# Optimization experiments

Measured on AMD Instinct MI355X. Metric: run time of the kernel, lower is better.

## Reference

```python
import jax, jax.numpy as jnp
import numpy as np

POPULATION = 1000000.0  # __init__ arg of MarkovChainRNN_Model
B, T, F = 16384, 2048, 2  # batch, timesteps, (beta, gamma) per step


def setup_inputs() -> dict:
    key = jax.random.key(0)
    k1, k2 = jax.random.split(key)
    # per-step (beta, gamma) rates in [0, 1)
    inputs = jax.random.uniform(k1, (B, T, F), dtype=jnp.float32)
    # initial [S, I, R] state; scaled so S+I+R is O(population)
    initial_state = jax.random.uniform(k2, (B, 3), dtype=jnp.float32) * POPULATION
    return {"inputs": inputs, "initial_state": initial_state}


def reference(inputs, initial_state):
    # SIR cell update, one step per day:
    #   new_inf = beta * S * I / N ; new_rec = gamma * I
    #   S' = S - new_inf ; I' = I + new_inf - new_rec ; R' = R + new_rec
    # Keras RNN(cell, return_state=True) -> (last_output, last_state);
    # for an SIR cell output == state, so both returns are the final state.
    def step(state, u):
        beta, gamma = u[:, 0], u[:, 1]            # [B], [B]
        S, I, R = state[:, 0], state[:, 1], state[:, 2]
        new_inf = beta * S * I / POPULATION
        new_rec = gamma * I
        new_state = jnp.stack([S - new_inf,
                               I + new_inf - new_rec,
                               R + new_rec], axis=-1)  # [B, 3]
        return new_state, None

    xs = jnp.transpose(inputs, (1, 0, 2))  # time-major [T, B, F]
    final_state, _ = jax.lax.scan(step, initial_state, xs)
    return (final_state, final_state)
```

## Files before the change

### kernel.cpp

```cpp
#include <hip/hip_runtime.h>
#include <stdint.h>
#include <stddef.h>


#define T_STEPS 2048
#define C_STEPS 64
#define NCHUNK  (T_STEPS / C_STEPS)
#define BPB     64
#define PAIRS   (C_STEPS / 2)
#define INSTR_PER_CHUNK 32

#define INV_POP 1e-6f

__device__ __forceinline__ void stage_chunk(const float* __restrict__ in,
                                            float4* lds, int b0, int c, int lane)
{
    const int hi = lane >> 5;
    const int q  = lane & 31;
#pragma unroll
    for (int j = 0; j < INSTR_PER_CHUNK; ++j) {
        const int bi = 2 * j + hi;
        const int p  = q ^ (bi & 15);
        const float* g = in
            + (size_t)(b0 + bi) * (T_STEPS * 2)
            + (size_t)c * (C_STEPS * 2)
            + (size_t)(p * 4);
        float4* l = lds + j * 64;
        __builtin_amdgcn_global_load_lds(
            (__attribute__((address_space(1))) void*)g,
            (__attribute__((address_space(3))) void*)l,
            16, 0, 0);
    }
}

__device__ __forceinline__ void compute_chunk(const float4* lds, int tid,
                                              float& S, float& I, float& R)
{
    const int swz = tid & 15;
    const float4* row = lds + tid * PAIRS;
#pragma unroll
    for (int p = 0; p < PAIRS; ++p) {
        const float4 v = row[p ^ swz];

        float ni = S * I * (v.x * INV_POP);
        float nr = v.y * I;
        S = S - ni;
        I = I + ni - nr;
        R = R + nr;

        ni = S * I * (v.z * INV_POP);
        nr = v.w * I;
        S = S - ni;
        I = I + ni - nr;
        R = R + nr;
    }
}

__global__ __launch_bounds__(64)
void sir_scan_kernel(const float* __restrict__ in, const float* __restrict__ init,
                     float* __restrict__ out, int half)
{
    __shared__ float4 bufA[BPB * PAIRS];
    __shared__ float4 bufB[BPB * PAIRS];

    const int tid = threadIdx.x;
    const int b0  = blockIdx.x * BPB;
    const int gb  = b0 + tid;

    float S = init[gb * 3 + 0];
    float I = init[gb * 3 + 1];
    float R = init[gb * 3 + 2];

    stage_chunk(in, bufA, b0, 0, tid);

#pragma unroll 1
    for (int c = 0; c < NCHUNK; c += 2) {
        asm volatile("s_waitcnt vmcnt(0)" ::: "memory");
        if (c + 1 < NCHUNK) stage_chunk(in, bufB, b0, c + 1, tid);
        compute_chunk(bufA, tid, S, I, R);

        asm volatile("s_waitcnt vmcnt(0)" ::: "memory");
        if (c + 2 < NCHUNK) stage_chunk(in, bufA, b0, c + 2, tid);
        compute_chunk(bufB, tid, S, I, R);
    }

    out[gb * 3 + 0] = S;
    out[gb * 3 + 1] = I;
    out[gb * 3 + 2] = R;
    out[half + gb * 3 + 0] = S;
    out[half + gb * 3 + 1] = I;
    out[half + gb * 3 + 2] = R;
}

extern "C" void kernel_launch(void* const* d_in, const int* in_sizes, int n_in,
                              void* d_out, int out_size, void* d_ws, size_t ws_size,
                              hipStream_t stream) {
    (void)in_sizes; (void)n_in; (void)d_ws; (void)ws_size;
    const float* in   = (const float*)d_in[0];
    const float* init = (const float*)d_in[1];
    float* out        = (float*)d_out;
    const int half = out_size / 2;

    dim3 grid(16384 / BPB);
    dim3 block(BPB);
    sir_scan_kernel<<<grid, block, 0, stream>>>(in, init, out, half);
}
```

Baseline: 61.83 us.

## Replace LDS staging with per-thread direct float4 loads triple-buffered in registers

Drops the cooperative global_load_lds staging into swizzled double-buffered LDS. Each thread now streams its own batch row with 128-byte float4 groups straight into registers, with three groups in flight to hide latency. This removes the LDS round trip and the full vmcnt(0) waits per chunk. In exchange, each load instruction now touches 64 scattered cache lines, one per lane, which may hurt coalescing and address-unit throughput. It also raises VGPR use.

```diff
diff --git a/kernel.cpp b/kernel.cpp
--- a/kernel.cpp
+++ b/kernel.cpp
@@ -4,43 +4,24 @@
 
 
 #define T_STEPS 2048
-#define C_STEPS 64
-#define NCHUNK  (T_STEPS / C_STEPS)
-#define BPB     64
-#define PAIRS   (C_STEPS / 2)
-#define INSTR_PER_CHUNK 32
-
+#define FPR     (T_STEPS * 2)
+#define NGROUP  128
 #define INV_POP 1e-6f
 
-__device__ __forceinline__ void stage_chunk(const float* __restrict__ in,
-                                            float4* lds, int b0, int c, int lane)
+__device__ __forceinline__ void load_group(const float4* __restrict__ row,
+                                           int idx, float4* g)
 {
-    const int hi = lane >> 5;
-    const int q  = lane & 31;
+    const float4* p = row + (size_t)idx * 8;
 #pragma unroll
-    for (int j = 0; j < INSTR_PER_CHUNK; ++j) {
-        const int bi = 2 * j + hi;
-        const int p  = q ^ (bi & 15);
-        const float* g = in
-            + (size_t)(b0 + bi) * (T_STEPS * 2)
-            + (size_t)c * (C_STEPS * 2)
-            + (size_t)(p * 4);
-        float4* l = lds + j * 64;
-        __builtin_amdgcn_global_load_lds(
-            (__attribute__((address_space(1))) void*)g,
-            (__attribute__((address_space(3))) void*)l,
-            16, 0, 0);
-    }
+    for (int j = 0; j < 8; ++j) g[j] = p[j];
 }
 
-__device__ __forceinline__ void compute_chunk(const float4* lds, int tid,
+__device__ __forceinline__ void compute_group(const float4* g,
                                               float& S, float& I, float& R)
 {
-    const int swz = tid & 15;
-    const float4* row = lds + tid * PAIRS;
 #pragma unroll
-    for (int p = 0; p < PAIRS; ++p) {
-        const float4 v = row[p ^ swz];
+    for (int j = 0; j < 8; ++j) {
+        const float4 v = g[j];
 
         float ni = S * I * (v.x * INV_POP);
         float nr = v.y * I;
@@ -60,29 +41,30 @@
 void sir_scan_kernel(const float* __restrict__ in, const float* __restrict__ init,
                      float* __restrict__ out, int half)
 {
-    __shared__ float4 bufA[BPB * PAIRS];
-    __shared__ float4 bufB[BPB * PAIRS];
-
     const int tid = threadIdx.x;
-    const int b0  = blockIdx.x * BPB;
-    const int gb  = b0 + tid;
+    const int gb  = blockIdx.x * 64 + tid;
+    const float4* row = (const float4*)(in + (size_t)gb * FPR);
 
     float S = init[gb * 3 + 0];
     float I = init[gb * 3 + 1];
     float R = init[gb * 3 + 2];
 
-    stage_chunk(in, bufA, b0, 0, tid);
+    float4 gA[8], gB[8], gC[8];
+    load_group(row, 0, gA);
+    load_group(row, 1, gB);
+    load_group(row, 2, gC);
 
 #pragma unroll 1
-    for (int c = 0; c < NCHUNK; c += 2) {
-        asm volatile("s_waitcnt vmcnt(0)" ::: "memory");
-        if (c + 1 < NCHUNK) stage_chunk(in, bufB, b0, c + 1, tid);
-        compute_chunk(bufA, tid, S, I, R);
-
-        asm volatile("s_waitcnt vmcnt(0)" ::: "memory");
-        if (c + 2 < NCHUNK) stage_chunk(in, bufA, b0, c + 2, tid);
-        compute_chunk(bufB, tid, S, I, R);
+    for (int k = 0; k < NGROUP - 2; k += 3) {
+        compute_group(gA, S, I, R);
+        { const int n = k + 3; load_group(row, n < NGROUP ? n : NGROUP - 1, gA); }
+        compute_group(gB, S, I, R);
+        { const int n = k + 4; load_group(row, n < NGROUP ? n : NGROUP - 1, gB); }
+        compute_group(gC, S, I, R);
+        { const int n = k + 5; load_group(row, n < NGROUP ? n : NGROUP - 1, gC); }
     }
+    compute_group(gA, S, I, R);
+    compute_group(gB, S, I, R);
 
     out[gb * 3 + 0] = S;
     out[gb * 3 + 1] = I;
@@ -101,7 +83,7 @@
     float* out        = (float*)d_out;
     const int half = out_size / 2;
 
-    dim3 grid(16384 / BPB);
-    dim3 block(BPB);
+    dim3 grid(16384 / 64);
+    dim3 block(64);
     sir_scan_kernel<<<grid, block, 0, stream>>>(in, init, out, half);
 }
```

New measurement: 115.6 us. 1.87x slower.
